# Kernel tuning notes

Hardware: AMD Instinct MI355X
Metric: run time of the kernel (lower is better)

Reference implementation:

```python
import jax, jax.numpy as jnp
import numpy as np

N = 50000   # nodes
E = 800000  # edges
D = 128     # input feature dim
H = 128     # hidden_channels
O = 128     # out_channels
NEG_SLOPE = 0.2


def setup_inputs() -> dict:
    key = jax.random.key(0)
    ks = jax.random.split(key, 16)
    x = jax.random.normal(ks[0], (N, D), dtype=jnp.float32)
    edge_idx = jax.random.randint(ks[1], (2, E), 0, N, dtype=jnp.int32)

    def lin(k, fin, fout):
        return jax.random.normal(k, (fin, fout), dtype=jnp.float32) / np.sqrt(fin)

    params = {
        # layer 1 (D -> H)
        "Wl1": lin(ks[2], D, H), "bl1": jnp.zeros((H,), jnp.float32),
        "Wr1": lin(ks[3], D, H), "br1": jnp.zeros((H,), jnp.float32),
        "att1": jax.random.normal(ks[4], (H,), dtype=jnp.float32) / np.sqrt(H),
        "b1": jnp.zeros((H,), jnp.float32),
        # layer 2 (H -> O)
        "Wl2": lin(ks[5], H, O), "bl2": jnp.zeros((O,), jnp.float32),
        "Wr2": lin(ks[6], H, O), "br2": jnp.zeros((O,), jnp.float32),
        "att2": jax.random.normal(ks[7], (O,), dtype=jnp.float32) / np.sqrt(O),
        "b2": jnp.zeros((O,), jnp.float32),
    }
    return {"x": x, "edge_idx": edge_idx, **params}


def gatv2_layer(x, src, dst, Wl, bl, Wr, br, att, bias):
    """Single-head GATv2Conv (add_self_loops=False), PyG semantics.

    message(x_j) uses lin_l(x_j); score uses leaky_relu(lin_l(x_j)+lin_r(x_i)) @ att,
    softmax over in-edges of each target node, scatter-add weighted messages.
    """
    xl = x @ Wl + bl            # [N, F] source transform
    xr = x @ Wr + br            # [N, F] target transform
    msg = xl[src]               # [E, F] gathered source messages
    e = jax.nn.leaky_relu(msg + xr[dst], NEG_SLOPE)  # [E, F]
    s = e @ att                 # [E] unnormalized scores
    smax = jax.lax.stop_gradient(jax.ops.segment_max(s, dst, num_segments=N))
    p = jnp.exp(s - smax[dst])  # stable segment softmax numerator
    denom = jax.ops.segment_sum(p, dst, num_segments=N)  # [N]
    alpha = p / denom[dst]      # [E]
    out = jax.ops.segment_sum(alpha[:, None] * msg, dst, num_segments=N)
    return out + bias


def reference(x, edge_idx, Wl1, bl1, Wr1, br1, att1, b1, Wl2, bl2, Wr2, br2, att2, b2):
    src, dst = edge_idx[0], edge_idx[1]
    h = jax.nn.relu(gatv2_layer(x, src, dst, Wl1, bl1, Wr1, br1, att1, b1))
    out = gatv2_layer(h, src, dst, Wl2, bl2, Wr2, br2, att2, b2)
    return out
```

## Files before the change

kernel.cpp:

```cpp
#include <hip/hip_runtime.h>
#include <math.h>


typedef short bf16x8 __attribute__((ext_vector_type(8)));
typedef float f32x4 __attribute__((ext_vector_type(4)));

__global__ __launch_bounds__(256) void count_prep_kernel(
    const int* __restrict__ dst, int* __restrict__ deg,
    unsigned short* __restrict__ rank16, int E, int nCnt,
    const float* __restrict__ W0, const float* __restrict__ W1,
    const float* __restrict__ W2, const float* __restrict__ W3,
    short* __restrict__ wt) {
    if ((int)blockIdx.x < nCnt) {
        int i = blockIdx.x * 256 + threadIdx.x;
        if (i < E) {
            int r = atomicAdd(&deg[dst[i]], 1);
            rank16[i] = (unsigned short)r;
        }
    } else {
        int b = blockIdx.x - nCnt;
        int mat = b >> 3, chunk = b & 7;
        const float* W = (mat == 0) ? W0 : (mat == 1) ? W1 : (mat == 2) ? W2 : W3;
        short* hi = wt + (size_t)mat * 2 * 16384;
        short* lo = hi + 16384;
        int i0 = chunk * 2048;
        for (int i = i0 + threadIdx.x; i < i0 + 2048; i += 256) {
            int k = i >> 7, n = i & 127;
            float x = W[i];
            unsigned u = __float_as_uint(x);
            unsigned hu = u & 0xFFFF0000u;
            float lf = x - __uint_as_float(hu);
            hi[n * 128 + k] = (short)(hu >> 16);
            lo[n * 128 + k] = (short)(__float_as_uint(lf) >> 16);
        }
    }
}

__global__ __launch_bounds__(256) void scan_blocksum_kernel(const int* __restrict__ deg,
                                                            int* __restrict__ blockSums, int n) {
    __shared__ int wsum[4];
    int tid = threadIdx.x;
    int idx = blockIdx.x * 256 + tid;
    int v = (idx < n) ? deg[idx] : 0;
    int lane = tid & 63, wid = tid >> 6;
    #pragma unroll
    for (int off = 32; off > 0; off >>= 1) v += __shfl_xor(v, off);
    if (lane == 0) wsum[wid] = v;
    __syncthreads();
    if (tid == 0) blockSums[blockIdx.x] = wsum[0] + wsum[1] + wsum[2] + wsum[3];
}

__global__ __launch_bounds__(256) void scan_apply2_kernel(
    const int* __restrict__ deg, const int* __restrict__ blockSums,
    int* __restrict__ row_ptr, int n, int nBlk) {
    __shared__ int sPre[4], sAll[4], wsum[4];
    int tid = threadIdx.x, lane = tid & 63, wid = tid >> 6;

    int bsv = (tid < nBlk) ? blockSums[tid] : 0;
    int pre = (tid < (int)blockIdx.x) ? bsv : 0;
    int all = bsv;
    #pragma unroll
    for (int off = 32; off > 0; off >>= 1) {
        pre += __shfl_xor(pre, off);
        all += __shfl_xor(all, off);
    }
    if (lane == 0) { sPre[wid] = pre; sAll[wid] = all; }
    __syncthreads();
    int off0 = sPre[0] + sPre[1] + sPre[2] + sPre[3];
    int total = sAll[0] + sAll[1] + sAll[2] + sAll[3];

    int idx = blockIdx.x * 256 + tid;
    int v = (idx < n) ? deg[idx] : 0;
    int incl = v;
    #pragma unroll
    for (int off = 1; off < 64; off <<= 1) {
        int t = __shfl_up(incl, off);
        if (lane >= off) incl += t;
    }
    if (lane == 63) wsum[wid] = incl;
    __syncthreads();
    int woff = 0;
    #pragma unroll
    for (int w = 0; w < 4; ++w) woff += (w < wid) ? wsum[w] : 0;
    int excl = off0 + woff + (incl - v);
    if (idx < n) row_ptr[idx] = excl;
    if (blockIdx.x == 0 && tid == 0) row_ptr[n] = total;
}

__global__ void scatter_edges_kernel(const int* __restrict__ src, const int* __restrict__ dst,
                                     const int* __restrict__ row_ptr,
                                     const unsigned short* __restrict__ rank16,
                                     unsigned short* __restrict__ csr16, int E) {
    int i = blockIdx.x * blockDim.x + threadIdx.x;
    if (i < E) {
        int d = dst[i];
        int pos = row_ptr[d] + (int)rank16[i];
        csr16[pos] = (unsigned short)src[i];
    }
}

#define LDK 136
__global__ __launch_bounds__(256) void gemm_mfma_dual32_kernel(
    const float* __restrict__ X, const short* __restrict__ wtL,
    const float* __restrict__ b0, short* __restrict__ out0bf,
    const float* __restrict__ b1, float* __restrict__ out1,
    int Nrows) {
    __shared__ __attribute__((aligned(16))) short Ahi[32][LDK];
    __shared__ __attribute__((aligned(16))) short Alo[32][LDK];

    int tid = threadIdx.x;
    int w = tid >> 6, lane = tid & 63, q = lane >> 4, tr = lane & 15;
    int m0 = blockIdx.x * 32;
    int n0 = w * 32;

    bf16x8 bh[4], bl[4];
    #pragma unroll
    for (int p = 0; p < 2; ++p) {
        const short* base = wtL + (size_t)p * 2 * 16384;
        #pragma unroll
        for (int nt = 0; nt < 2; ++nt) {
            size_t boff = (size_t)(n0 + nt * 16 + tr) * 128 + q * 8;
            bh[p * 2 + nt] = *(const bf16x8*)&base[boff];
            bl[p * 2 + nt] = *(const bf16x8*)&base[16384 + boff];
        }
    }

    {
        int srow = tid >> 3;
        int c0 = (tid & 7) * 16;
        int gr = m0 + srow; if (gr >= Nrows) gr = Nrows - 1;
        const float* xp = &X[(size_t)gr * 128 + c0];
        float4 v[4];
        #pragma unroll
        for (int j = 0; j < 4; ++j) v[j] = *(const float4*)(xp + j * 4);
        #pragma unroll
        for (int j = 0; j < 2; ++j) {
            bf16x8 hv, lv;
            #pragma unroll
            for (int k = 0; k < 2; ++k) {
                float4 vv = v[j * 2 + k];
                float f[4] = {vv.x, vv.y, vv.z, vv.w};
                #pragma unroll
                for (int e = 0; e < 4; ++e) {
                    unsigned u = __float_as_uint(f[e]);
                    unsigned hu = u & 0xFFFF0000u;
                    float lf = f[e] - __uint_as_float(hu);
                    hv[k * 4 + e] = (short)(hu >> 16);
                    lv[k * 4 + e] = (short)(__float_as_uint(lf) >> 16);
                }
            }
            *(bf16x8*)&Ahi[srow][c0 + j * 8] = hv;
            *(bf16x8*)&Alo[srow][c0 + j * 8] = lv;
        }
    }
    __syncthreads();

    f32x4 acc[2][4];
    #pragma unroll
    for (int a = 0; a < 2; ++a)
        #pragma unroll
        for (int b = 0; b < 4; ++b) acc[a][b] = (f32x4){0.f, 0.f, 0.f, 0.f};

    for (int kc = 0; kc < 128; kc += 32) {
        #pragma unroll
        for (int mt = 0; mt < 2; ++mt) {
            bf16x8 ah = *(const bf16x8*)&Ahi[mt * 16 + tr][kc + q * 8];
            bf16x8 al = *(const bf16x8*)&Alo[mt * 16 + tr][kc + q * 8];
            #pragma unroll
            for (int j = 0; j < 4; ++j) {
                acc[mt][j] = __builtin_amdgcn_mfma_f32_16x16x32_bf16(ah, bh[j], acc[mt][j], 0, 0, 0);
                acc[mt][j] = __builtin_amdgcn_mfma_f32_16x16x32_bf16(ah, bl[j], acc[mt][j], 0, 0, 0);
                acc[mt][j] = __builtin_amdgcn_mfma_f32_16x16x32_bf16(al, bh[j], acc[mt][j], 0, 0, 0);
            }
        }
        if (kc < 96) {
            #pragma unroll
            for (int p = 0; p < 2; ++p) {
                const short* base = wtL + (size_t)p * 2 * 16384;
                #pragma unroll
                for (int nt = 0; nt < 2; ++nt) {
                    size_t boff = (size_t)(n0 + nt * 16 + tr) * 128 + (kc + 32) + q * 8;
                    bh[p * 2 + nt] = *(const bf16x8*)&base[boff];
                    bl[p * 2 + nt] = *(const bf16x8*)&base[16384 + boff];
                }
            }
        }
    }

    #pragma unroll
    for (int nt = 0; nt < 2; ++nt) {
        float bv0 = b0[n0 + nt * 16 + tr];
        float bv1 = b1[n0 + nt * 16 + tr];
        #pragma unroll
        for (int mt = 0; mt < 2; ++mt) {
            #pragma unroll
            for (int r = 0; r < 4; ++r) {
                int row = m0 + mt * 16 + q * 4 + r;
                if (row < Nrows) {
                    float v0 = acc[mt][nt][r] + bv0;
                    unsigned u = __float_as_uint(v0);
                    unsigned rb = (u + 0x7FFFu + ((u >> 16) & 1u)) >> 16;
                    out0bf[(size_t)row * 128 + n0 + nt * 16 + tr] = (short)rb;
                    out1[(size_t)row * 128 + n0 + nt * 16 + tr] = acc[mt][2 + nt][r] + bv1;
                }
            }
        }
    }
}
#undef LDK

__global__ __launch_bounds__(256) void gat_aggregate_kernel(
    const short* __restrict__ xl16, const float* __restrict__ xr,
    const float* __restrict__ att, const float* __restrict__ bias,
    const int* __restrict__ row_ptr, const unsigned short* __restrict__ csr16,
    float* __restrict__ out, int N, int applyRelu) {
    int wid = threadIdx.x >> 6;
    int lane = threadIdx.x & 63;
    int qlane = lane & 15;
    int qid = lane >> 4;
    int node = blockIdx.x * 4 + wid;
    if (node >= N) return;

    const bf16x8* xlb = (const bf16x8*)xl16;
    float4 xrA = ((const float4*)xr)[(size_t)node * 32 + qlane * 2];
    float4 xrB = ((const float4*)xr)[(size_t)node * 32 + qlane * 2 + 1];
    float4 atA = ((const float4*)att)[qlane * 2];
    float4 atB = ((const float4*)att)[qlane * 2 + 1];

    int beg = row_ptr[node];
    int end = row_ptr[node + 1];

    float dsum = 0.f;
    float4 accA = {0.f, 0.f, 0.f, 0.f};
    float4 accB = {0.f, 0.f, 0.f, 0.f};

    for (int cbase = beg; cbase < end; cbase += 64) {
        int cnt = end - cbase;
        if (cnt > 64) cnt = 64;
        int myidx = (lane < cnt) ? (int)csr16[cbase + lane] : 0;
        int nq = (cnt + 3) >> 2;

        for (int g = 0; g < nq; ++g) {
            int eidx = 4 * g + qid;
            int s = __shfl(myidx, eidx);
            bf16x8 mv = xlb[((size_t)s << 4) + qlane];
            float4 vA, vB;
            vA.x = __uint_as_float(((unsigned)(unsigned short)mv[0]) << 16);
            vA.y = __uint_as_float(((unsigned)(unsigned short)mv[1]) << 16);
            vA.z = __uint_as_float(((unsigned)(unsigned short)mv[2]) << 16);
            vA.w = __uint_as_float(((unsigned)(unsigned short)mv[3]) << 16);
            vB.x = __uint_as_float(((unsigned)(unsigned short)mv[4]) << 16);
            vB.y = __uint_as_float(((unsigned)(unsigned short)mv[5]) << 16);
            vB.z = __uint_as_float(((unsigned)(unsigned short)mv[6]) << 16);
            vB.w = __uint_as_float(((unsigned)(unsigned short)mv[7]) << 16);

            float t, p;
            t = vA.x + xrA.x; t = t > 0.f ? t : 0.2f * t; p = t * atA.x;
            t = vA.y + xrA.y; t = t > 0.f ? t : 0.2f * t; p = fmaf(t, atA.y, p);
            t = vA.z + xrA.z; t = t > 0.f ? t : 0.2f * t; p = fmaf(t, atA.z, p);
            t = vA.w + xrA.w; t = t > 0.f ? t : 0.2f * t; p = fmaf(t, atA.w, p);
            t = vB.x + xrB.x; t = t > 0.f ? t : 0.2f * t; p = fmaf(t, atB.x, p);
            t = vB.y + xrB.y; t = t > 0.f ? t : 0.2f * t; p = fmaf(t, atB.y, p);
            t = vB.z + xrB.z; t = t > 0.f ? t : 0.2f * t; p = fmaf(t, atB.z, p);
            t = vB.w + xrB.w; t = t > 0.f ? t : 0.2f * t; p = fmaf(t, atB.w, p);

            p += __shfl_xor(p, 1);
            p += __shfl_xor(p, 2);
            p += __shfl_xor(p, 4);
            p += __shfl_xor(p, 8);

            float e = (eidx < cnt) ? __expf(p) : 0.f;
            dsum += e;
            accA.x = fmaf(e, vA.x, accA.x);
            accA.y = fmaf(e, vA.y, accA.y);
            accA.z = fmaf(e, vA.z, accA.z);
            accA.w = fmaf(e, vA.w, accA.w);
            accB.x = fmaf(e, vB.x, accB.x);
            accB.y = fmaf(e, vB.y, accB.y);
            accB.z = fmaf(e, vB.z, accB.z);
            accB.w = fmaf(e, vB.w, accB.w);
        }
    }

    #pragma unroll
    for (int off = 16; off <= 32; off <<= 1) {
        dsum += __shfl_xor(dsum, off);
        accA.x += __shfl_xor(accA.x, off);
        accA.y += __shfl_xor(accA.y, off);
        accA.z += __shfl_xor(accA.z, off);
        accA.w += __shfl_xor(accA.w, off);
        accB.x += __shfl_xor(accB.x, off);
        accB.y += __shfl_xor(accB.y, off);
        accB.z += __shfl_xor(accB.z, off);
        accB.w += __shfl_xor(accB.w, off);
    }

    float inv = dsum > 0.f ? 1.f / dsum : 0.f;
    float4 bvA = ((const float4*)bias)[qlane * 2];
    float4 bvB = ((const float4*)bias)[qlane * 2 + 1];
    float4 oA, oB;
    oA.x = accA.x * inv + bvA.x; oA.y = accA.y * inv + bvA.y;
    oA.z = accA.z * inv + bvA.z; oA.w = accA.w * inv + bvA.w;
    oB.x = accB.x * inv + bvB.x; oB.y = accB.y * inv + bvB.y;
    oB.z = accB.z * inv + bvB.z; oB.w = accB.w * inv + bvB.w;
    if (applyRelu) {
        oA.x = fmaxf(oA.x, 0.f); oA.y = fmaxf(oA.y, 0.f);
        oA.z = fmaxf(oA.z, 0.f); oA.w = fmaxf(oA.w, 0.f);
        oB.x = fmaxf(oB.x, 0.f); oB.y = fmaxf(oB.y, 0.f);
        oB.z = fmaxf(oB.z, 0.f); oB.w = fmaxf(oB.w, 0.f);
    }
    if (lane < 16) {
        ((float4*)out)[(size_t)node * 32 + qlane * 2] = oA;
        ((float4*)out)[(size_t)node * 32 + qlane * 2 + 1] = oB;
    }
}


extern "C" void kernel_launch(void* const* d_in, const int* in_sizes, int n_in,
                              void* d_out, int out_size, void* d_ws, size_t ws_size,
                              hipStream_t stream) {
    const float* x    = (const float*)d_in[0];
    const int* eidx   = (const int*)d_in[1];
    const float* Wl1  = (const float*)d_in[2];
    const float* bl1  = (const float*)d_in[3];
    const float* Wr1  = (const float*)d_in[4];
    const float* br1  = (const float*)d_in[5];
    const float* att1 = (const float*)d_in[6];
    const float* b1   = (const float*)d_in[7];
    const float* Wl2  = (const float*)d_in[8];
    const float* bl2  = (const float*)d_in[9];
    const float* Wr2  = (const float*)d_in[10];
    const float* br2  = (const float*)d_in[11];
    const float* att2 = (const float*)d_in[12];
    const float* b2   = (const float*)d_in[13];

    const int N = in_sizes[0] / 128;
    const int E = in_sizes[1] / 2;
    const int* src = eidx;
    const int* dst = eidx + E;

    const int nBlk = (N + 255) / 256;

    size_t NF = (size_t)N * 128;
    short* xl16 = (short*)d_ws;
    float* bufB = (float*)(xl16 + NF);
    float* bufC = bufB + NF;
    int* deg       = (int*)(bufC + NF);
    int* row_ptr   = deg + N;
    int* blockSums = row_ptr + (N + 1);
    unsigned short* rank16 = (unsigned short*)(blockSums + nBlk);
    unsigned short* csr16  = rank16 + E;
    short* wt      = (short*)(csr16 + E);

    float* outF = (float*)d_out;

    const int nCnt = (E + 255) / 256;
    hipMemsetAsync(deg, 0, (size_t)N * sizeof(int), stream);
    count_prep_kernel<<<nCnt + 32, 256, 0, stream>>>(dst, deg, rank16, E, nCnt,
                                                     Wl1, Wr1, Wl2, Wr2, wt);
    scan_blocksum_kernel<<<nBlk, 256, 0, stream>>>(deg, blockSums, N);
    scan_apply2_kernel<<<nBlk, 256, 0, stream>>>(deg, blockSums, row_ptr, N, nBlk);
    scatter_edges_kernel<<<nCnt, 256, 0, stream>>>(src, dst, row_ptr, rank16, csr16, E);

    dim3 gemmGrid((N + 31) / 32);
    dim3 aggGrid((N + 3) / 4);

    gemm_mfma_dual32_kernel<<<gemmGrid, 256, 0, stream>>>(x, wt, bl1, xl16, br1, bufB, N);
    gat_aggregate_kernel<<<aggGrid, 256, 0, stream>>>(xl16, bufB, att1, b1, row_ptr, csr16,
                                                      bufC, N, 1);
    gemm_mfma_dual32_kernel<<<gemmGrid, 256, 0, stream>>>(bufC, wt + 2 * 2 * 16384, bl2, xl16,
                                                          br2, bufB, N);
    gat_aggregate_kernel<<<aggGrid, 256, 0, stream>>>(xl16, bufB, att2, b2, row_ptr, csr16,
                                                      outF, N, 0);
}
```

Measured before the change: 301.9 us.

## Split degree-count atomics into 8 slices to reduce contention, use fmaxf leaky relu

Degree counting now uses 8 separate per-slice count arrays, selected by block index, so the atomic adds on popular destinations are spread across copies. The scan computes a per-slice base offset for each node and per-slice row pointers, and the scatter uses the slice's row pointer. This adds an 8N memset, extra reads and writes in the scan kernels, and more workspace. Separately, leaky ReLU in the aggregate is rewritten as fmaxf(t, 0.2t) to avoid a select.

```diff
diff --git a/kernel.cpp b/kernel.cpp
--- a/kernel.cpp
+++ b/kernel.cpp
@@ -6,15 +6,16 @@
 typedef float f32x4 __attribute__((ext_vector_type(4)));
 
 __global__ __launch_bounds__(256) void count_prep_kernel(
-    const int* __restrict__ dst, int* __restrict__ deg,
-    unsigned short* __restrict__ rank16, int E, int nCnt,
+    const int* __restrict__ dst, int* __restrict__ deg8,
+    unsigned short* __restrict__ rank16, int E, int N, int nCnt,
     const float* __restrict__ W0, const float* __restrict__ W1,
     const float* __restrict__ W2, const float* __restrict__ W3,
     short* __restrict__ wt) {
     if ((int)blockIdx.x < nCnt) {
         int i = blockIdx.x * 256 + threadIdx.x;
         if (i < E) {
-            int r = atomicAdd(&deg[dst[i]], 1);
+            int slice = blockIdx.x & 7;
+            int r = atomicAdd(&deg8[(size_t)slice * N + dst[i]], 1);
             rank16[i] = (unsigned short)r;
         }
     } else {
@@ -36,13 +37,26 @@
     }
 }
 
-__global__ __launch_bounds__(256) void scan_blocksum_kernel(const int* __restrict__ deg,
-                                                            int* __restrict__ blockSums, int n) {
+__global__ __launch_bounds__(256) void scan_blocksum2_kernel(
+    const int* __restrict__ deg8, unsigned short* __restrict__ base8,
+    int* __restrict__ dtot, int* __restrict__ blockSums, int n) {
     __shared__ int wsum[4];
     int tid = threadIdx.x;
     int idx = blockIdx.x * 256 + tid;
-    int v = (idx < n) ? deg[idx] : 0;
     int lane = tid & 63, wid = tid >> 6;
+    int tot = 0;
+    if (idx < n) {
+        int b = 0;
+        #pragma unroll
+        for (int s = 0; s < 8; ++s) {
+            int v = deg8[(size_t)s * n + idx];
+            base8[(size_t)s * n + idx] = (unsigned short)b;
+            b += v;
+        }
+        tot = b;
+        dtot[idx] = tot;
+    }
+    int v = tot;
     #pragma unroll
     for (int off = 32; off > 0; off >>= 1) v += __shfl_xor(v, off);
     if (lane == 0) wsum[wid] = v;
@@ -51,8 +65,9 @@
 }
 
 __global__ __launch_bounds__(256) void scan_apply2_kernel(
-    const int* __restrict__ deg, const int* __restrict__ blockSums,
-    int* __restrict__ row_ptr, int n, int nBlk) {
+    const int* __restrict__ dtot, const int* __restrict__ blockSums,
+    const unsigned short* __restrict__ base8,
+    int* __restrict__ row_ptr, int* __restrict__ rpb, int n, int nBlk) {
     __shared__ int sPre[4], sAll[4], wsum[4];
     int tid = threadIdx.x, lane = tid & 63, wid = tid >> 6;
 
@@ -70,7 +85,7 @@
     int total = sAll[0] + sAll[1] + sAll[2] + sAll[3];
 
     int idx = blockIdx.x * 256 + tid;
-    int v = (idx < n) ? deg[idx] : 0;
+    int v = (idx < n) ? dtot[idx] : 0;
     int incl = v;
     #pragma unroll
     for (int off = 1; off < 64; off <<= 1) {
@@ -83,18 +98,24 @@
     #pragma unroll
     for (int w = 0; w < 4; ++w) woff += (w < wid) ? wsum[w] : 0;
     int excl = off0 + woff + (incl - v);
-    if (idx < n) row_ptr[idx] = excl;
+    if (idx < n) {
+        row_ptr[idx] = excl;
+        #pragma unroll
+        for (int s = 0; s < 8; ++s)
+            rpb[(size_t)s * n + idx] = excl + (int)base8[(size_t)s * n + idx];
+    }
     if (blockIdx.x == 0 && tid == 0) row_ptr[n] = total;
 }
 
 __global__ void scatter_edges_kernel(const int* __restrict__ src, const int* __restrict__ dst,
-                                     const int* __restrict__ row_ptr,
+                                     const int* __restrict__ rpb,
                                      const unsigned short* __restrict__ rank16,
-                                     unsigned short* __restrict__ csr16, int E) {
+                                     unsigned short* __restrict__ csr16, int E, int N) {
     int i = blockIdx.x * blockDim.x + threadIdx.x;
     if (i < E) {
         int d = dst[i];
-        int pos = row_ptr[d] + (int)rank16[i];
+        int slice = blockIdx.x & 7;
+        int pos = rpb[(size_t)slice * N + d] + (int)rank16[i];
         csr16[pos] = (unsigned short)src[i];
     }
 }
@@ -255,14 +276,14 @@
             vB.w = __uint_as_float(((unsigned)(unsigned short)mv[7]) << 16);
 
             float t, p;
-            t = vA.x + xrA.x; t = t > 0.f ? t : 0.2f * t; p = t * atA.x;
-            t = vA.y + xrA.y; t = t > 0.f ? t : 0.2f * t; p = fmaf(t, atA.y, p);
-            t = vA.z + xrA.z; t = t > 0.f ? t : 0.2f * t; p = fmaf(t, atA.z, p);
-            t = vA.w + xrA.w; t = t > 0.f ? t : 0.2f * t; p = fmaf(t, atA.w, p);
-            t = vB.x + xrB.x; t = t > 0.f ? t : 0.2f * t; p = fmaf(t, atB.x, p);
-            t = vB.y + xrB.y; t = t > 0.f ? t : 0.2f * t; p = fmaf(t, atB.y, p);
-            t = vB.z + xrB.z; t = t > 0.f ? t : 0.2f * t; p = fmaf(t, atB.z, p);
-            t = vB.w + xrB.w; t = t > 0.f ? t : 0.2f * t; p = fmaf(t, atB.w, p);
+            t = vA.x + xrA.x; t = fmaxf(t, 0.2f * t); p = t * atA.x;
+            t = vA.y + xrA.y; t = fmaxf(t, 0.2f * t); p = fmaf(t, atA.y, p);
+            t = vA.z + xrA.z; t = fmaxf(t, 0.2f * t); p = fmaf(t, atA.z, p);
+            t = vA.w + xrA.w; t = fmaxf(t, 0.2f * t); p = fmaf(t, atA.w, p);
+            t = vB.x + xrB.x; t = fmaxf(t, 0.2f * t); p = fmaf(t, atB.x, p);
+            t = vB.y + xrB.y; t = fmaxf(t, 0.2f * t); p = fmaf(t, atB.y, p);
+            t = vB.z + xrB.z; t = fmaxf(t, 0.2f * t); p = fmaf(t, atB.z, p);
+            t = vB.w + xrB.w; t = fmaxf(t, 0.2f * t); p = fmaf(t, atB.w, p);
 
             p += __shfl_xor(p, 1);
             p += __shfl_xor(p, 2);
@@ -345,22 +366,25 @@
     short* xl16 = (short*)d_ws;
     float* bufB = (float*)(xl16 + NF);
     float* bufC = bufB + NF;
-    int* deg       = (int*)(bufC + NF);
-    int* row_ptr   = deg + N;
+    int* deg8      = (int*)(bufC + NF);
+    int* dtot      = deg8 + 8 * (size_t)N;
+    int* row_ptr   = dtot + N;
     int* blockSums = row_ptr + (N + 1);
-    unsigned short* rank16 = (unsigned short*)(blockSums + nBlk);
+    int* rpb       = blockSums + nBlk;
+    unsigned short* base8  = (unsigned short*)(rpb + 8 * (size_t)N);
+    unsigned short* rank16 = base8 + 8 * (size_t)N;
     unsigned short* csr16  = rank16 + E;
     short* wt      = (short*)(csr16 + E);
 
     float* outF = (float*)d_out;
 
     const int nCnt = (E + 255) / 256;
-    hipMemsetAsync(deg, 0, (size_t)N * sizeof(int), stream);
-    count_prep_kernel<<<nCnt + 32, 256, 0, stream>>>(dst, deg, rank16, E, nCnt,
+    hipMemsetAsync(deg8, 0, 8 * (size_t)N * sizeof(int), stream);
+    count_prep_kernel<<<nCnt + 32, 256, 0, stream>>>(dst, deg8, rank16, E, N, nCnt,
                                                      Wl1, Wr1, Wl2, Wr2, wt);
-    scan_blocksum_kernel<<<nBlk, 256, 0, stream>>>(deg, blockSums, N);
-    scan_apply2_kernel<<<nBlk, 256, 0, stream>>>(deg, blockSums, row_ptr, N, nBlk);
-    scatter_edges_kernel<<<nCnt, 256, 0, stream>>>(src, dst, row_ptr, rank16, csr16, E);
+    scan_blocksum2_kernel<<<nBlk, 256, 0, stream>>>(deg8, base8, dtot, blockSums, N);
+    scan_apply2_kernel<<<nBlk, 256, 0, stream>>>(dtot, blockSums, base8, row_ptr, rpb, N, nBlk);
+    scatter_edges_kernel<<<nCnt, 256, 0, stream>>>(src, dst, rpb, rank16, csr16, E, N);
 
     dim3 gemmGrid((N + 31) / 32);
     dim3 aggGrid((N + 3) / 4);
```

Measured after the change: 296.7 us. No clear change (-1.7%).
